# Kernel tuning notes

Hardware: AMD Instinct MI355X
Metric: run time of the kernel (lower is better)

Reference implementation:

```python
import jax, jax.numpy as jnp
import numpy as np

B, H, W, C = 4, 256, 256, 64
KH = KW = 3
UNITS = 1          # forced: conv in-channels must equal kernel in-channels (see notes)
G = 1              # num_deformable_group
HP, WP = H + 2, W + 2  # 'same' padding for 3x3 stride-1: pad 1 each side


def _conv_indices(h, w):
    """Replicates tf.image.extract_image_patches('SAME') on an index grid:
    border patches read zero-padded coordinates. Returns int [h, w, 9]."""
    yg, xg = jnp.meshgrid(jnp.arange(h), jnp.arange(w), indexing='ij')
    yp = jnp.pad(yg, 1)
    xp = jnp.pad(xg, 1)
    ys = jnp.stack([yp[ky:ky + h, kx:kx + w] for ky in range(KH) for kx in range(KW)], -1)
    xs = jnp.stack([xp[ky:ky + h, kx:kx + w] for ky in range(KH) for kx in range(KW)], -1)
    return ys, xs


def setup_inputs() -> dict:
    key = jax.random.key(0)
    k1, k2, k3, k4 = jax.random.split(key, 4)
    input_fp = jax.random.normal(k1, (B, H, W, C), jnp.float32)
    gt_mask = jax.random.randint(k2, (1, H, W, 1), 0, 2).astype(jnp.float32)
    offset = jax.random.normal(k3, (B, H, W, UNITS * KH * KW * 2), jnp.float32)
    fan_in = KH * KW * C
    kernel = jax.random.normal(k4, (KH, KW, C, UNITS), jnp.float32) / np.float32(np.sqrt(fan_in))
    bias = jnp.zeros((UNITS,), jnp.float32)
    return {"input_fp": input_fp, "gt_mask": gt_mask, "offset": offset,
            "kernel": kernel, "bias": bias}


def reference(input_fp, gt_mask, offset, kernel, bias):
    pad = ((0, 0), (1, 1), (1, 1), (0, 0))
    fp = jnp.pad(input_fp, pad)                 # [B, HP, WP, C]
    mk = jnp.pad(gt_mask, pad)[0, :, :, 0]      # [HP, WP]; original tiles this over batch/channels

    off = offset.reshape(B, H, W, UNITS * KH * KW, 2)
    y_off, x_off = off[..., 0], off[..., 1]     # [B, H, W, 9]

    yi, xi = _conv_indices(H, W)                # [H, W, 9] int
    yf = yi[None].astype(jnp.float32)           # [1, H, W, 9], broadcasts over batch
    xf = xi[None].astype(jnp.float32)

    # mask at base sample points and at offset sample points
    p_mask = mk[yi, xi][None]                                        # [1, H, W, 9]
    yo = jnp.clip(jnp.floor(yf + y_off).astype(jnp.int32), 0, HP - 1)
    xo = jnp.clip(jnp.floor(xf + x_off).astype(jnp.int32), 0, WP - 1)
    p_mask_off = mk[yo, xo]                                          # [B, H, W, 9]
    diff = (p_mask != p_mask_off).astype(jnp.float32)

    y = jnp.clip(yf + y_off * diff, 0.0, H - 1.0)
    x = jnp.clip(xf + x_off * diff, 0.0, W - 1.0)
    y0 = jnp.floor(y).astype(jnp.int32)
    x0 = jnp.floor(x).astype(jnp.int32)

    b = jnp.arange(B)[:, None, None, None]
    pixels = fp[b, y0, x0]                      # [B, H, W, 9, C] nearest-floor sampling
    # [B,H,W,kh,kw,G,C] -> [B,H,kh,W,kw,G,C] -> [B, H*kh, W*kw, G*C]
    pixels = pixels.reshape(B, H, W, KH, KW, G, C)
    pixels = pixels.transpose(0, 1, 3, 2, 4, 5, 6)
    pixels = pixels.reshape(B, H * KH, W * KW, G * C)   # feat_in_group = units//G = 1, tile is a no-op

    out = jax.lax.conv_general_dilated(
        pixels, kernel, window_strides=(KH, KW), padding='SAME',
        dimension_numbers=('NHWC', 'HWIO', 'NHWC'))      # [B, H, W, UNITS]
    return out + bias
```

## Files before the change

### kernel.cpp

```cpp
#include <hip/hip_runtime.h>

#define HW 256
#define CH 64

__global__ __launch_bounds__(256, 6) void DeformableConvLayer_kernel(
    const float* __restrict__ inp,
    const float* __restrict__ gt,
    const float* __restrict__ off,
    const float* __restrict__ ker,
    const float* __restrict__ bias,
    float* __restrict__ out)
{
    __shared__ float wlds[576];
    const int tid = threadIdx.x;
    if (tid < 144) ((float4*)wlds)[tid] = ((const float4*)ker)[tid];

    const int lane = tid & 63;
    const int wave = tid >> 6;
    const int q16  = lane & 48;
    const int t    = lane & 15;

    const int bid = blockIdx.x;
    const int vb  = (bid & 7) * 2048 + (bid >> 3);

    const int p = vb * 16 + wave * 4 + (q16 >> 4);
    const int b = p >> 16;
    const int i = (p >> 8) & 255;
    const int j = p & 255;
    const float* inb = inp + (long)b * (HW * HW * CH);

    int pack = 0;
    if (t < 9) {
        const int tap = t;
        const int ky = tap / 3, kx = tap - ky * 3;
        int iy = i + ky - 1, ix = j + kx - 1;
        bool interior = (iy >= 0) & (iy < HW) & (ix >= 0) & (ix < HW);
        int yi = interior ? iy : 0;
        int xi = interior ? ix : 0;

        float p_mask = (yi >= 1 && xi >= 1) ? gt[(yi - 1) * HW + (xi - 1)] : 0.f;

        float2 o2 = *(const float2*)(off + (long)p * 18 + 2 * tap);
        float yf = (float)yi, xf = (float)xi;

        float yof = fminf(fmaxf(floorf(yf + o2.x), 0.f), 257.f);
        float xof = fminf(fmaxf(floorf(xf + o2.y), 0.f), 257.f);
        int yo = (int)yof, xo = (int)xof;
        float p_mask_off = (yo >= 1 && yo <= HW && xo >= 1 && xo <= HW)
                           ? gt[(yo - 1) * HW + (xo - 1)] : 0.f;
        float diff = (p_mask != p_mask_off) ? 1.f : 0.f;

        float y = fminf(fmaxf(yf + o2.x * diff, 0.f), 255.f);
        float x = fminf(fmaxf(xf + o2.y * diff, 0.f), 255.f);
        int y0 = (int)y;
        int x0 = (int)x;

        bool valid = (y0 >= 1) & (x0 >= 1);
        int eoff = ((y0 - 1) * HW + (x0 - 1)) * CH;
        pack = valid ? eoff : -1;
    }

    int pk[9];
    #pragma unroll
    for (int k = 0; k < 9; ++k) pk[k] = __shfl(pack, q16 + k);

    float4 v[9];
    #pragma unroll
    for (int k = 0; k < 9; ++k) {
        int eo = pk[k] >= 0 ? pk[k] : 0;
        v[k] = *(const float4*)(inb + eo + t * 4);
    }

    __syncthreads();

    float acc = 0.f;
    #pragma unroll
    for (int k = 0; k < 9; ++k) {
        float s = pk[k] >= 0 ? 1.f : 0.f;
        float4 w = ((const float4*)wlds)[k * 16 + t];
        float d = v[k].x * w.x + v[k].y * w.y + v[k].z * w.z + v[k].w * w.w;
        acc = fmaf(s, d, acc);
    }

    acc += __shfl_xor(acc, 8);
    acc += __shfl_xor(acc, 4);
    acc += __shfl_xor(acc, 2);
    acc += __shfl_xor(acc, 1);
    if (t == 0) out[p] = acc + bias[0];
}

extern "C" void kernel_launch(void* const* d_in, const int* in_sizes, int n_in,
                              void* d_out, int out_size, void* d_ws, size_t ws_size,
                              hipStream_t stream) {
    const float* inp  = (const float*)d_in[0];
    const float* gt   = (const float*)d_in[1];
    const float* off  = (const float*)d_in[2];
    const float* ker  = (const float*)d_in[3];
    const float* bias = (const float*)d_in[4];
    float* out = (float*)d_out;

    DeformableConvLayer_kernel<<<16384, 256, 0, stream>>>(inp, gt, off, ker, bias, out);
}
```

Baseline: 133.1 us.

## Process two output pixels per 16-lane group with LDS tap offsets and DPP reduction

Each 16-lane group now handles two output pixels, so the grid is halved and 18 gathers per thread are in flight instead of 9. Tap offsets are exchanged through LDS instead of cross-lane shuffles. The final reduction uses DPP row rotates. Occupancy bound drops from 6 to 4 to leave room for the extra registers, and the added barrier before the gathers could reduce overlap.

```diff
diff --git a/kernel.cpp b/kernel.cpp
--- a/kernel.cpp
+++ b/kernel.cpp
@@ -3,7 +3,43 @@
 #define HW 256
 #define CH 64
 
-__global__ __launch_bounds__(256, 6) void DeformableConvLayer_kernel(
+template <int CTRL>
+__device__ __forceinline__ float row_rot_add(float v) {
+    int r = __builtin_amdgcn_update_dpp(0, __float_as_int(v), CTRL, 0xf, 0xf, false);
+    return v + __int_as_float(r);
+}
+
+__device__ __forceinline__ int tap_pack(const float* __restrict__ gt,
+                                        const float* __restrict__ off,
+                                        int p, int i, int j, int tap) {
+    int ky = tap / 3, kx = tap - ky * 3;
+    int iy = i + ky - 1, ix = j + kx - 1;
+    bool interior = (iy >= 0) & (iy < HW) & (ix >= 0) & (ix < HW);
+    int yi = interior ? iy : 0;
+    int xi = interior ? ix : 0;
+
+    float p_mask = (yi >= 1 && xi >= 1) ? gt[(yi - 1) * HW + (xi - 1)] : 0.f;
+
+    float2 o2 = *(const float2*)(off + (long)p * 18 + 2 * tap);
+    float yf = (float)yi, xf = (float)xi;
+
+    float yof = fminf(fmaxf(floorf(yf + o2.x), 0.f), 257.f);
+    float xof = fminf(fmaxf(floorf(xf + o2.y), 0.f), 257.f);
+    int yo = (int)yof, xo = (int)xof;
+    float p_mask_off = (yo >= 1 && yo <= HW && xo >= 1 && xo <= HW)
+                       ? gt[(yo - 1) * HW + (xo - 1)] : 0.f;
+    float diff = (p_mask != p_mask_off) ? 1.f : 0.f;
+
+    float y = fminf(fmaxf(yf + o2.x * diff, 0.f), 255.f);
+    float x = fminf(fmaxf(xf + o2.y * diff, 0.f), 255.f);
+    int y0 = (int)y, x0 = (int)x;
+
+    bool valid = (y0 >= 1) & (x0 >= 1);
+    int eoff = ((y0 - 1) * HW + (x0 - 1)) * CH;
+    return valid ? eoff : -1;
+}
+
+__global__ __launch_bounds__(256, 4) void DeformableConvLayer_kernel(
     const float* __restrict__ inp,
     const float* __restrict__ gt,
     const float* __restrict__ off,
@@ -12,81 +48,76 @@
     float* __restrict__ out)
 {
     __shared__ float wlds[576];
+    __shared__ int   pklds[4][2][4][12];
+
     const int tid = threadIdx.x;
     if (tid < 144) ((float4*)wlds)[tid] = ((const float4*)ker)[tid];
 
     const int lane = tid & 63;
     const int wave = tid >> 6;
-    const int q16  = lane & 48;
+    const int q    = lane >> 4;
     const int t    = lane & 15;
 
     const int bid = blockIdx.x;
-    const int vb  = (bid & 7) * 2048 + (bid >> 3);
+    const int vb  = (bid & 7) * 1024 + (bid >> 3);
 
-    const int p = vb * 16 + wave * 4 + (q16 >> 4);
-    const int b = p >> 16;
-    const int i = (p >> 8) & 255;
-    const int j = p & 255;
+    const int base = vb * 32 + wave * 8;
+    const int pA = base + q;
+    const int pB = base + 4 + q;
+    const int b  = base >> 16;
     const float* inb = inp + (long)b * (HW * HW * CH);
 
-    int pack = 0;
     if (t < 9) {
-        const int tap = t;
-        const int ky = tap / 3, kx = tap - ky * 3;
-        int iy = i + ky - 1, ix = j + kx - 1;
-        bool interior = (iy >= 0) & (iy < HW) & (ix >= 0) & (ix < HW);
-        int yi = interior ? iy : 0;
-        int xi = interior ? ix : 0;
+        int iA = (pA >> 8) & 255, jA = pA & 255;
+        int iB = (pB >> 8) & 255, jB = pB & 255;
+        pklds[wave][0][q][t] = tap_pack(gt, off, pA, iA, jA, t);
+        pklds[wave][1][q][t] = tap_pack(gt, off, pB, iB, jB, t);
+    }
+    __syncthreads();
 
-        float p_mask = (yi >= 1 && xi >= 1) ? gt[(yi - 1) * HW + (xi - 1)] : 0.f;
+    int pkA[9], pkB[9];
+    #pragma unroll
+    for (int k = 0; k < 9; ++k) pkA[k] = pklds[wave][0][q][k];
+    #pragma unroll
+    for (int k = 0; k < 9; ++k) pkB[k] = pklds[wave][1][q][k];
 
-        float2 o2 = *(const float2*)(off + (long)p * 18 + 2 * tap);
-        float yf = (float)yi, xf = (float)xi;
+    float4 vA[9], vB[9];
+    #pragma unroll
+    for (int k = 0; k < 9; ++k) {
+        int eo = pkA[k] >= 0 ? pkA[k] : 0;
+        vA[k] = *(const float4*)(inb + eo + t * 4);
+    }
+    #pragma unroll
+    for (int k = 0; k < 9; ++k) {
+        int eo = pkB[k] >= 0 ? pkB[k] : 0;
+        vB[k] = *(const float4*)(inb + eo + t * 4);
+    }
+    asm volatile("" ::: "memory");
 
-        float yof = fminf(fmaxf(floorf(yf + o2.x), 0.f), 257.f);
-        float xof = fminf(fmaxf(floorf(xf + o2.y), 0.f), 257.f);
-        int yo = (int)yof, xo = (int)xof;
-        float p_mask_off = (yo >= 1 && yo <= HW && xo >= 1 && xo <= HW)
-                           ? gt[(yo - 1) * HW + (xo - 1)] : 0.f;
-        float diff = (p_mask != p_mask_off) ? 1.f : 0.f;
-
-        float y = fminf(fmaxf(yf + o2.x * diff, 0.f), 255.f);
-        float x = fminf(fmaxf(xf + o2.y * diff, 0.f), 255.f);
-        int y0 = (int)y;
-        int x0 = (int)x;
-
-        bool valid = (y0 >= 1) & (x0 >= 1);
-        int eoff = ((y0 - 1) * HW + (x0 - 1)) * CH;
-        pack = valid ? eoff : -1;
+    float accA = 0.f, accB = 0.f;
+    #pragma unroll
+    for (int k = 0; k < 9; ++k) {
+        float4 w = ((const float4*)wlds)[k * 16 + t];
+        float dA = vA[k].x * w.x + vA[k].y * w.y + vA[k].z * w.z + vA[k].w * w.w;
+        float dB = vB[k].x * w.x + vB[k].y * w.y + vB[k].z * w.z + vB[k].w * w.w;
+        accA = fmaf(pkA[k] >= 0 ? 1.f : 0.f, dA, accA);
+        accB = fmaf(pkB[k] >= 0 ? 1.f : 0.f, dB, accB);
     }
 
-    int pk[9];
-    #pragma unroll
-    for (int k = 0; k < 9; ++k) pk[k] = __shfl(pack, q16 + k);
+    accA = row_rot_add<0x128>(accA);
+    accA = row_rot_add<0x124>(accA);
+    accA = row_rot_add<0x122>(accA);
+    accA = row_rot_add<0x121>(accA);
+    accB = row_rot_add<0x128>(accB);
+    accB = row_rot_add<0x124>(accB);
+    accB = row_rot_add<0x122>(accB);
+    accB = row_rot_add<0x121>(accB);
 
-    float4 v[9];
-    #pragma unroll
-    for (int k = 0; k < 9; ++k) {
-        int eo = pk[k] >= 0 ? pk[k] : 0;
-        v[k] = *(const float4*)(inb + eo + t * 4);
+    if (t == 0) {
+        float bs = bias[0];
+        out[pA] = accA + bs;
+        out[pB] = accB + bs;
     }
-
-    __syncthreads();
-
-    float acc = 0.f;
-    #pragma unroll
-    for (int k = 0; k < 9; ++k) {
-        float s = pk[k] >= 0 ? 1.f : 0.f;
-        float4 w = ((const float4*)wlds)[k * 16 + t];
-        float d = v[k].x * w.x + v[k].y * w.y + v[k].z * w.z + v[k].w * w.w;
-        acc = fmaf(s, d, acc);
-    }
-
-    acc += __shfl_xor(acc, 8);
-    acc += __shfl_xor(acc, 4);
-    acc += __shfl_xor(acc, 2);
-    acc += __shfl_xor(acc, 1);
-    if (t == 0) out[p] = acc + bias[0];
 }
 
 extern "C" void kernel_launch(void* const* d_in, const int* in_sizes, int n_in,
@@ -99,5 +130,5 @@
     const float* bias = (const float*)d_in[4];
     float* out = (float*)d_out;
 
-    DeformableConvLayer_kernel<<<16384, 256, 0, stream>>>(inp, gt, off, ker, bias, out);
+    DeformableConvLayer_kernel<<<8192, 256, 0, stream>>>(inp, gt, off, ker, bias, out);
 }
```

New measurement: 139.4 us. +4.7%, slower.

## Software-pipeline deformable sampling across pixel groups per wave with DPP reductions

Applied to the files above, without the earlier changes.

Each wave now handles 8 groups of 4 output pixels instead of one, using a four-stage software pipeline (offset load, mask lookups, gather, dot product) separated by sched_barriers. This lets the dependent global loads of different groups overlap. Kernel weights are kept in registers instead of LDS, which removes the __syncthreads. The shuffle-xor reduction is replaced with DPP row rotations. The grid shrinks 8x and launch bounds drop to 3 waves per SIMD, so register pressure rises and occupancy falls.

```diff
diff --git a/kernel.cpp b/kernel.cpp
--- a/kernel.cpp
+++ b/kernel.cpp
@@ -2,8 +2,17 @@
 
 #define HW 256
 #define CH 64
+#define NG 8
+#define NPX (NG * 4)
+#define LASTP 262143
 
-__global__ __launch_bounds__(256, 6) void DeformableConvLayer_kernel(
+template <int CTRL>
+__device__ __forceinline__ float row_rot_add(float v) {
+    int r = __builtin_amdgcn_update_dpp(0, __float_as_int(v), CTRL, 0xf, 0xf, false);
+    return v + __int_as_float(r);
+}
+
+__global__ __launch_bounds__(256, 3) void DeformableConvLayer_kernel(
     const float* __restrict__ inp,
     const float* __restrict__ gt,
     const float* __restrict__ off,
@@ -11,82 +20,107 @@
     const float* __restrict__ bias,
     float* __restrict__ out)
 {
-    __shared__ float wlds[576];
-    const int tid = threadIdx.x;
-    if (tid < 144) ((float4*)wlds)[tid] = ((const float4*)ker)[tid];
-
+    const int tid  = threadIdx.x;
     const int lane = tid & 63;
     const int wave = tid >> 6;
-    const int q16  = lane & 48;
+    const int q    = lane >> 4;
     const int t    = lane & 15;
+    const int tp   = t < 9 ? t : 8;
+    const int ky   = tp / 3, kx = tp - ky * 3;
+    const int grpbase = lane & 48;
 
     const int bid = blockIdx.x;
-    const int vb  = (bid & 7) * 2048 + (bid >> 3);
+    const int vb  = (bid & 7) * 256 + (bid >> 3);
+    const int wbase = (vb * 4 + wave) * NPX;
+    const int b = wbase >> 16;
+    const float* inb = inp + (long)b * (HW * HW * CH);
+    const float bs = bias[0];
 
-    const int p = vb * 16 + wave * 4 + (q16 >> 4);
-    const int b = p >> 16;
-    const int i = (p >> 8) & 255;
-    const int j = p & 255;
-    const float* inb = inp + (long)b * (HW * HW * CH);
+    float4 w[9];
+    #pragma unroll
+    for (int k = 0; k < 9; ++k)
+        w[k] = *(const float4*)(ker + k * CH + t * 4);
 
-    int pack = 0;
-    if (t < 9) {
-        const int tap = t;
-        const int ky = tap / 3, kx = tap - ky * 3;
+    float o2y[2], o2x[2];
+    float pmask[2], pmoff[2], cy[2], cx[2], yfb[2], xfb[2];
+    float4 v[2][9];
+    int smask[2];
+
+    auto S1 = [&](int gg, int B) {
+        int p = wbase + gg * 4 + q; p = p > LASTP ? LASTP : p;
+        float2 o = *(const float2*)(off + (long)p * 18 + 2 * tp);
+        o2y[B] = o.x; o2x[B] = o.y;
+    };
+
+    auto S2 = [&](int gg, int B) {
+        int p = wbase + gg * 4 + q; p = p > LASTP ? LASTP : p;
+        int i = (p >> 8) & 255, j = p & 255;
         int iy = i + ky - 1, ix = j + kx - 1;
         bool interior = (iy >= 0) & (iy < HW) & (ix >= 0) & (ix < HW);
         int yi = interior ? iy : 0;
         int xi = interior ? ix : 0;
+        float yf = (float)yi, xf = (float)xi;
+        yfb[B] = yf; xfb[B] = xf;
+        pmask[B] = (yi >= 1 && xi >= 1) ? gt[(yi - 1) * HW + (xi - 1)] : 0.f;
+        float oy = o2y[B], ox = o2x[B];
+        float yof = fminf(fmaxf(floorf(yf + oy), 0.f), 257.f);
+        float xof = fminf(fmaxf(floorf(xf + ox), 0.f), 257.f);
+        int yo = (int)yof, xo = (int)xof;
+        pmoff[B] = (yo >= 1 && yo <= HW && xo >= 1 && xo <= HW)
+                   ? gt[(yo - 1) * HW + (xo - 1)] : 0.f;
+        cy[B] = fminf(fmaxf(yf + oy, 0.f), 255.f);
+        cx[B] = fminf(fmaxf(xf + ox, 0.f), 255.f);
+    };
 
-        float p_mask = (yi >= 1 && xi >= 1) ? gt[(yi - 1) * HW + (xi - 1)] : 0.f;
+    auto S3 = [&](int gg, int B) {
+        bool diff = (pmask[B] != pmoff[B]);
+        float y = diff ? cy[B] : yfb[B];
+        float x = diff ? cx[B] : xfb[B];
+        int y0 = (int)y, x0 = (int)x;
+        bool valid = (y0 >= 1) & (x0 >= 1);
+        int pack = valid ? ((y0 - 1) * HW + (x0 - 1)) * CH : -1;
+        int m = 0;
+        #pragma unroll
+        for (int k = 0; k < 9; ++k) {
+            int pk = __shfl(pack, grpbase + k);
+            m |= (pk >= 0 ? 1 : 0) << k;
+            int eo = pk >= 0 ? pk : 0;
+            v[B][k] = *(const float4*)(inb + eo + t * 4);
+        }
+        smask[B] = m;
+    };
 
-        float2 o2 = *(const float2*)(off + (long)p * 18 + 2 * tap);
-        float yf = (float)yi, xf = (float)xi;
+    auto S4 = [&](int gg, int B) {
+        float acc = 0.f;
+        int m = smask[B];
+        #pragma unroll
+        for (int k = 0; k < 9; ++k) {
+            float4 vv = v[B][k];
+            float d = vv.x * w[k].x + vv.y * w[k].y + vv.z * w[k].z + vv.w * w[k].w;
+            float s = (float)((m >> k) & 1);
+            acc = fmaf(s, d, acc);
+        }
+        acc = row_rot_add<0x128>(acc);
+        acc = row_rot_add<0x124>(acc);
+        acc = row_rot_add<0x122>(acc);
+        acc = row_rot_add<0x121>(acc);
+        if (t == 0) out[wbase + gg * 4 + q] = acc + bs;
+    };
 
-        float yof = fminf(fmaxf(floorf(yf + o2.x), 0.f), 257.f);
-        float xof = fminf(fmaxf(floorf(xf + o2.y), 0.f), 257.f);
-        int yo = (int)yof, xo = (int)xof;
-        float p_mask_off = (yo >= 1 && yo <= HW && xo >= 1 && xo <= HW)
-                           ? gt[(yo - 1) * HW + (xo - 1)] : 0.f;
-        float diff = (p_mask != p_mask_off) ? 1.f : 0.f;
+    S1(0, 0);
+    __builtin_amdgcn_sched_barrier(0);
+    S1(1, 1); S2(0, 0);
+    __builtin_amdgcn_sched_barrier(0);
+    S1(2, 0); S2(1, 1); S3(0, 0);
+    __builtin_amdgcn_sched_barrier(0);
 
-        float y = fminf(fmaxf(yf + o2.x * diff, 0.f), 255.f);
-        float x = fminf(fmaxf(xf + o2.y * diff, 0.f), 255.f);
-        int y0 = (int)y;
-        int x0 = (int)x;
-
-        bool valid = (y0 >= 1) & (x0 >= 1);
-        int eoff = ((y0 - 1) * HW + (x0 - 1)) * CH;
-        pack = valid ? eoff : -1;
+    #pragma unroll
+    for (int n = 0; n < NG; n += 2) {
+        S1(n + 3, 1); S2(n + 2, 0); S3(n + 1, 1); S4(n, 0);
+        __builtin_amdgcn_sched_barrier(0);
+        S1(n + 4, 0); S2(n + 3, 1); S3(n + 2, 0); S4(n + 1, 1);
+        __builtin_amdgcn_sched_barrier(0);
     }
-
-    int pk[9];
-    #pragma unroll
-    for (int k = 0; k < 9; ++k) pk[k] = __shfl(pack, q16 + k);
-
-    float4 v[9];
-    #pragma unroll
-    for (int k = 0; k < 9; ++k) {
-        int eo = pk[k] >= 0 ? pk[k] : 0;
-        v[k] = *(const float4*)(inb + eo + t * 4);
-    }
-
-    __syncthreads();
-
-    float acc = 0.f;
-    #pragma unroll
-    for (int k = 0; k < 9; ++k) {
-        float s = pk[k] >= 0 ? 1.f : 0.f;
-        float4 w = ((const float4*)wlds)[k * 16 + t];
-        float d = v[k].x * w.x + v[k].y * w.y + v[k].z * w.z + v[k].w * w.w;
-        acc = fmaf(s, d, acc);
-    }
-
-    acc += __shfl_xor(acc, 8);
-    acc += __shfl_xor(acc, 4);
-    acc += __shfl_xor(acc, 2);
-    acc += __shfl_xor(acc, 1);
-    if (t == 0) out[p] = acc + bias[0];
 }
 
 extern "C" void kernel_launch(void* const* d_in, const int* in_sizes, int n_in,
@@ -99,5 +133,5 @@
     const float* bias = (const float*)d_in[4];
     float* out = (float*)d_out;
 
-    DeformableConvLayer_kernel<<<16384, 256, 0, stream>>>(inp, gt, off, ker, bias, out);
+    DeformableConvLayer_kernel<<<2048, 256, 0, stream>>>(inp, gt, off, ker, bias, out);
 }
```

After: 134.3 us. Within noise of the previous version (+0.9%).

## Split index computation into separate kernel and use DPP row reduction

Applied to the files above, without the earlier changes.

Moves the per-tap offset/mask index computation into its own fully parallel kernel that writes packed gather offsets to workspace. The gather kernel then reads the offsets, loads weights straight from global memory instead of staging them in LDS (dropping the barrier), and reduces with DPP row rotates instead of shuffles. The aim is to stop 7 of every 16 lanes idling during index math and to shorten the gather kernel. In exchange it adds a second launch plus a workspace write and read of 2.4M ints.

```diff
diff --git a/kernel.cpp b/kernel.cpp
--- a/kernel.cpp
+++ b/kernel.cpp
@@ -3,66 +3,76 @@
 #define HW 256
 #define CH 64
 
-__global__ __launch_bounds__(256, 6) void DeformableConvLayer_kernel(
-    const float* __restrict__ inp,
+template <int CTRL>
+__device__ __forceinline__ float row_rot_add(float v) {
+    int r = __builtin_amdgcn_update_dpp(0, __float_as_int(v), CTRL, 0xf, 0xf, false);
+    return v + __int_as_float(r);
+}
+
+__global__ __launch_bounds__(256) void dcl_index_kernel(
     const float* __restrict__ gt,
     const float* __restrict__ off,
+    int* __restrict__ ws)
+{
+    unsigned u = blockIdx.x * 256 + threadIdx.x;
+    unsigned p = __umulhi(u, 0x38E38E39u) >> 1;
+    int tap = u - p * 9;
+    int i = (p >> 8) & 255, j = p & 255;
+    int ky = tap / 3, kx = tap - ky * 3;
+
+    float2 o2 = *(const float2*)(off + 2ul * u);
+
+    int iy = i + ky - 1, ix = j + kx - 1;
+    bool interior = (iy >= 0) & (iy < HW) & (ix >= 0) & (ix < HW);
+    int yi = interior ? iy : 0;
+    int xi = interior ? ix : 0;
+    float yf = (float)yi, xf = (float)xi;
+
+    float p_mask = (yi >= 1 && xi >= 1) ? gt[(yi - 1) * HW + (xi - 1)] : 0.f;
+
+    float yof = fminf(fmaxf(floorf(yf + o2.x), 0.f), 257.f);
+    float xof = fminf(fmaxf(floorf(xf + o2.y), 0.f), 257.f);
+    int yo = (int)yof, xo = (int)xof;
+    float p_mask_off = (yo >= 1 && yo <= HW && xo >= 1 && xo <= HW)
+                       ? gt[(yo - 1) * HW + (xo - 1)] : 0.f;
+    float diff = (p_mask != p_mask_off) ? 1.f : 0.f;
+
+    float y = fminf(fmaxf(yf + o2.x * diff, 0.f), 255.f);
+    float x = fminf(fmaxf(xf + o2.y * diff, 0.f), 255.f);
+    int y0 = (int)y, x0 = (int)x;
+
+    bool valid = (y0 >= 1) & (x0 >= 1);
+    ws[u] = valid ? ((y0 - 1) * HW + (x0 - 1)) * CH : -1;
+}
+
+__global__ __launch_bounds__(256) void dcl_gather_kernel(
+    const float* __restrict__ inp,
+    const int*   __restrict__ ws,
     const float* __restrict__ ker,
     const float* __restrict__ bias,
     float* __restrict__ out)
 {
-    __shared__ float wlds[576];
-    const int tid = threadIdx.x;
-    if (tid < 144) ((float4*)wlds)[tid] = ((const float4*)ker)[tid];
-
+    const int tid  = threadIdx.x;
     const int lane = tid & 63;
     const int wave = tid >> 6;
-    const int q16  = lane & 48;
+    const int q    = lane >> 4;
     const int t    = lane & 15;
 
     const int bid = blockIdx.x;
     const int vb  = (bid & 7) * 2048 + (bid >> 3);
 
-    const int p = vb * 16 + wave * 4 + (q16 >> 4);
+    const int p = vb * 16 + wave * 4 + q;
     const int b = p >> 16;
-    const int i = (p >> 8) & 255;
-    const int j = p & 255;
     const float* inb = inp + (long)b * (HW * HW * CH);
-
-    int pack = 0;
-    if (t < 9) {
-        const int tap = t;
-        const int ky = tap / 3, kx = tap - ky * 3;
-        int iy = i + ky - 1, ix = j + kx - 1;
-        bool interior = (iy >= 0) & (iy < HW) & (ix >= 0) & (ix < HW);
-        int yi = interior ? iy : 0;
-        int xi = interior ? ix : 0;
-
-        float p_mask = (yi >= 1 && xi >= 1) ? gt[(yi - 1) * HW + (xi - 1)] : 0.f;
-
-        float2 o2 = *(const float2*)(off + (long)p * 18 + 2 * tap);
-        float yf = (float)yi, xf = (float)xi;
-
-        float yof = fminf(fmaxf(floorf(yf + o2.x), 0.f), 257.f);
-        float xof = fminf(fmaxf(floorf(xf + o2.y), 0.f), 257.f);
-        int yo = (int)yof, xo = (int)xof;
-        float p_mask_off = (yo >= 1 && yo <= HW && xo >= 1 && xo <= HW)
-                           ? gt[(yo - 1) * HW + (xo - 1)] : 0.f;
-        float diff = (p_mask != p_mask_off) ? 1.f : 0.f;
-
-        float y = fminf(fmaxf(yf + o2.x * diff, 0.f), 255.f);
-        float x = fminf(fmaxf(xf + o2.y * diff, 0.f), 255.f);
-        int y0 = (int)y;
-        int x0 = (int)x;
-
-        bool valid = (y0 >= 1) & (x0 >= 1);
-        int eoff = ((y0 - 1) * HW + (x0 - 1)) * CH;
-        pack = valid ? eoff : -1;
-    }
 
     int pk[9];
     #pragma unroll
-    for (int k = 0; k < 9; ++k) pk[k] = __shfl(pack, q16 + k);
+    for (int k = 0; k < 9; ++k) pk[k] = ws[p * 9 + k];
+
+    float4 w[9];
+    #pragma unroll
+    for (int k = 0; k < 9; ++k)
+        w[k] = *(const float4*)(ker + k * CH + t * 4);
 
     float4 v[9];
     #pragma unroll
@@ -71,21 +81,19 @@
         v[k] = *(const float4*)(inb + eo + t * 4);
     }
 
-    __syncthreads();
-
     float acc = 0.f;
     #pragma unroll
     for (int k = 0; k < 9; ++k) {
-        float s = pk[k] >= 0 ? 1.f : 0.f;
-        float4 w = ((const float4*)wlds)[k * 16 + t];
-        float d = v[k].x * w.x + v[k].y * w.y + v[k].z * w.z + v[k].w * w.w;
-        acc = fmaf(s, d, acc);
+        float d = v[k].x * w[k].x + v[k].y * w[k].y
+                + v[k].z * w[k].z + v[k].w * w[k].w;
+        acc = fmaf(pk[k] >= 0 ? 1.f : 0.f, d, acc);
     }
 
-    acc += __shfl_xor(acc, 8);
-    acc += __shfl_xor(acc, 4);
-    acc += __shfl_xor(acc, 2);
-    acc += __shfl_xor(acc, 1);
+    acc = row_rot_add<0x128>(acc);
+    acc = row_rot_add<0x124>(acc);
+    acc = row_rot_add<0x122>(acc);
+    acc = row_rot_add<0x121>(acc);
+
     if (t == 0) out[p] = acc + bias[0];
 }
 
@@ -98,6 +106,8 @@
     const float* ker  = (const float*)d_in[3];
     const float* bias = (const float*)d_in[4];
     float* out = (float*)d_out;
+    int* ws = (int*)d_ws;
 
-    DeformableConvLayer_kernel<<<16384, 256, 0, stream>>>(inp, gt, off, ker, bias, out);
+    dcl_index_kernel<<<9216, 256, 0, stream>>>(gt, off, ws);
+    dcl_gather_kernel<<<16384, 256, 0, stream>>>(inp, ws, ker, bias, out);
 }
```

After: 154.6 us. 16.2% more time.
